# Performance work log

Measured on AMD Instinct MI355X. Metric: run time of the kernel, lower is better.

The kernel has to match this reference:

```python
import math
import jax, jax.numpy as jnp
import numpy as np

B_SZ, N_TOK, D_MODEL, EXPAND, D_STATE = 4, 1024, 192, 2, 16
D_INNER = EXPAND * D_MODEL  # 384


def setup_inputs() -> dict:
    key = jax.random.key(0)
    ks = jax.random.split(key, 6)
    dt_init = math.log(math.exp(0.1) - 1.0)
    x = jax.random.normal(ks[0], (B_SZ, N_TOK, D_INNER), dtype=jnp.float32)
    # dt projection weights: uniform(-1e-4, 1e-4), bias = softplus-inverse(0.1)
    W_dts = jax.random.uniform(ks[1], (D_INNER, D_INNER), minval=-1e-4, maxval=1e-4, dtype=jnp.float32)
    W_dtd = jax.random.uniform(ks[2], (D_INNER, D_INNER), minval=-1e-4, maxval=1e-4, dtype=jnp.float32)
    b_dts = jnp.full((D_INNER,), dt_init, dtype=jnp.float32)
    b_dtd = jnp.full((D_INNER,), dt_init, dtype=jnp.float32)
    # B/C projections (no bias)
    W_B = jax.random.normal(ks[3], (D_STATE, D_INNER), dtype=jnp.float32) * 0.05
    W_C = jax.random.normal(ks[4], (D_STATE, D_INNER), dtype=jnp.float32) * 0.05
    D_param = jnp.ones((D_INNER,), dtype=jnp.float32)
    A_log = jnp.broadcast_to(jnp.log(jnp.arange(1, D_STATE + 1, dtype=jnp.float32))[None, :], (D_INNER, D_STATE))
    diff_raw = jnp.zeros((1, D_INNER, 1, 1), dtype=jnp.float32)
    return {"x": x, "W_dts": W_dts, "b_dts": b_dts, "W_dtd": W_dtd, "b_dtd": b_dtd,
            "W_B": W_B, "W_C": W_C, "D_param": D_param, "A_log": A_log,
            "diff_raw": diff_raw, "K_steps": 3}


def _laplacian(h, H, W):
    # h: (B, N, D, S); 5-point stencil with replicate (edge) padding, per (D,S) channel
    Bv, N, D, S = h.shape
    g = h.reshape(Bv, H, W, D, S)
    g = jnp.pad(g, ((0, 0), (1, 1), (1, 1), (0, 0), (0, 0)), mode='edge')
    lap = (g[:, 2:, 1:-1] + g[:, :-2, 1:-1] + g[:, 1:-1, 2:] + g[:, 1:-1, :-2]
           - 4.0 * g[:, 1:-1, 1:-1])
    return lap.reshape(Bv, N, D, S)


def reference(x, W_dts, b_dts, W_dtd, b_dtd, W_B, W_C, D_param, A_log, diff_raw, K_steps):
    Bv, N, D = x.shape
    H = Wd = int(math.sqrt(N))
    A = -jax.nn.softplus(A_log)                                   # (D, S), negative decay
    delta_s = jnp.minimum(jax.nn.softplus(x @ W_dts.T + b_dts), 0.15)  # (B, N, D)
    delta_d = jnp.minimum(jax.nn.softplus(x @ W_dtd.T + b_dtd), 0.15)  # (B, N, D)
    B_mat = x @ W_B.T                                             # (B, N, S)
    C_mat = x @ W_C.T                                             # (B, N, S)
    h0 = jnp.einsum('bnd,bns->bnds', x, B_mat)                    # (B, N, D, S)
    D_coeff = (jax.nn.sigmoid(diff_raw) * 0.5).reshape(1, 1, D, 1)
    dt = 1.0 / K_steps
    A_exp = A[None, None]            # (1, 1, D, S)
    ds_e = delta_s[..., None]        # (B, N, D, 1)
    dd_e = delta_d[..., None]
    h = h0
    for _ in range(K_steps):
        lap = _laplacian(h, H, Wd)
        h = h + dt * (ds_e * (A_exp * h + h0) + dd_e * D_coeff * lap)
    y = jnp.einsum('bnds,bns->bnd', h, C_mat) + x * D_param
    return y
```

## Files before the change

### kernel.cpp

```cpp
#include <hip/hip_runtime.h>
#include <hip/hip_bf16.h>

#define BSZ   4
#define NTOK  1024
#define DIN   384
#define DST   16
#define MROWS (BSZ * NTOK)
#define KDIM  384
#define NM    (MROWS * DIN)

typedef __attribute__((ext_vector_type(8))) short bf16x8;
typedef __attribute__((ext_vector_type(4))) float f32x4;

__device__ __forceinline__ float softplus_f(float z) {
  return (z > 20.0f) ? z : log1pf(expf(z));
}

__device__ __forceinline__ unsigned short f32_to_bf16(float f) {
  unsigned int u = __float_as_uint(f);
  unsigned int rnd = 0x7fffu + ((u >> 16) & 1u);
  return (unsigned short)((u + rnd) >> 16);
}

__device__ __forceinline__ float bf16_lo(unsigned int w) { return __uint_as_float(w << 16); }
__device__ __forceinline__ float bf16_hi(unsigned int w) { return __uint_as_float(w & 0xffff0000u); }

__global__ __launch_bounds__(256) void wconv_kernel(
    const float* __restrict__ Wdts, const float* __restrict__ Wdtd,
    const float* __restrict__ WB,   const float* __restrict__ WC,
    unsigned short* __restrict__ Wb)
{
  const int idx8 = (blockIdx.x * 256 + threadIdx.x) * 8;
  const int row = idx8 / KDIM;
  const int k   = idx8 % KDIM;
  uint4 o = make_uint4(0u, 0u, 0u, 0u);
  if (row < 800) {
    const float* src;
    if (row < 384)      src = Wdts + (long)row * KDIM + k;
    else if (row < 768) src = Wdtd + (long)(row - 384) * KDIM + k;
    else if (row < 784) src = WB   + (long)(row - 768) * KDIM + k;
    else                src = WC   + (long)(row - 784) * KDIM + k;
    float4 v0 = *(const float4*)src;
    float4 v1 = *(const float4*)(src + 4);
    o.x = (unsigned int)f32_to_bf16(v0.x) | ((unsigned int)f32_to_bf16(v0.y) << 16);
    o.y = (unsigned int)f32_to_bf16(v0.z) | ((unsigned int)f32_to_bf16(v0.w) << 16);
    o.z = (unsigned int)f32_to_bf16(v1.x) | ((unsigned int)f32_to_bf16(v1.y) << 16);
    o.w = (unsigned int)f32_to_bf16(v1.z) | ((unsigned int)f32_to_bf16(v1.w) << 16);
  }
  *(uint4*)&Wb[idx8] = o;
}

__global__ __launch_bounds__(256) void xpose_kernel(
    const float* __restrict__ x, float* __restrict__ xT,
    unsigned short* __restrict__ xb)
{
  __shared__ float tile[32][33];
  const int n0 = blockIdx.x * 32;
  const int d0 = blockIdx.y * 32;
  const int b  = blockIdx.z;
  const int tx = threadIdx.x & 31, ty = threadIdx.x >> 5;
#pragma unroll
  for (int i = 0; i < 4; ++i) {
    int nn = n0 + ty + i * 8;
    float v = x[(long)(b * NTOK + nn) * DIN + d0 + tx];
    tile[ty + i * 8][tx] = v;
    xb[(long)(b * NTOK + nn) * DIN + d0 + tx] = f32_to_bf16(v);
  }
  __syncthreads();
#pragma unroll
  for (int i = 0; i < 4; ++i) {
    int dd = d0 + ty + i * 8;
    xT[(long)(b * DIN + dd) * NTOK + n0 + tx] = tile[tx][ty + i * 8];
  }
}

__global__ __launch_bounds__(256) void proj_mfma_kernel(
    const unsigned short* __restrict__ xb,
    const unsigned short* __restrict__ Wb,
    const float* __restrict__ bdts, const float* __restrict__ bdtd,
    unsigned short* __restrict__ dsT, unsigned short* __restrict__ ddT,
    float* __restrict__ BT, float* __restrict__ CT)
{
  __shared__ short smem_s[2][2][64 * 72];

  const int t    = threadIdx.x;
  const int bm   = blockIdx.x & 63;
  const int bn   = blockIdx.x >> 6;
  const int row0 = bm * 64;
  const int col0 = bn * 64;
  const int bat  = row0 >> 10;
  const int n0   = row0 & 1023;

  const int l  = t & 63;
  const int w  = t >> 6;
  const int wr = (w >> 1) * 32;
  const int wc = (w & 1) * 32;
  const int lr = l & 15;
  const int lk = (l >> 4) * 8;

  const int sr = t >> 2;
  const int sk = (t & 3) * 16;

  f32x4 acc[2][2];
  const f32x4 zero = {0.f, 0.f, 0.f, 0.f};
  acc[0][0] = zero; acc[0][1] = zero; acc[1][0] = zero; acc[1][1] = zero;

  uint4 la0, la1, lw0, lw1;
#define PLOAD(K0)                                                          \
  {                                                                        \
    const unsigned short* ap = &xb[(long)(row0 + sr) * KDIM + (K0) + sk];  \
    const unsigned short* wp = &Wb[(long)(col0 + sr) * KDIM + (K0) + sk];  \
    la0 = *(const uint4*)ap;  la1 = *(const uint4*)(ap + 8);               \
    lw0 = *(const uint4*)wp;  lw1 = *(const uint4*)(wp + 8);               \
  }
#define PSTORE(BUF)                                                        \
  {                                                                        \
    *(uint4*)&smem_s[BUF][0][sr * 72 + sk]     = la0;                      \
    *(uint4*)&smem_s[BUF][0][sr * 72 + sk + 8] = la1;                      \
    *(uint4*)&smem_s[BUF][1][sr * 72 + sk]     = lw0;                      \
    *(uint4*)&smem_s[BUF][1][sr * 72 + sk + 8] = lw1;                      \
  }

  PLOAD(0);
  PSTORE(0);

  for (int it = 0; it < 6; ++it) {
    const int cur = it & 1;
    __syncthreads();
    if (it + 1 < 6) PLOAD((it + 1) * 64);
    const short* Asm = smem_s[cur][0];
    const short* Wsm = smem_s[cur][1];
#pragma unroll
    for (int kh = 0; kh < 2; ++kh) {
      const int ko = kh * 32 + lk;
      bf16x8 a0 = *(const bf16x8*)&Asm[(wr + lr) * 72 + ko];
      bf16x8 a1 = *(const bf16x8*)&Asm[(wr + 16 + lr) * 72 + ko];
      bf16x8 b0 = *(const bf16x8*)&Wsm[(wc + lr) * 72 + ko];
      bf16x8 b1 = *(const bf16x8*)&Wsm[(wc + 16 + lr) * 72 + ko];
      acc[0][0] = __builtin_amdgcn_mfma_f32_16x16x32_bf16(a0, b0, acc[0][0], 0, 0, 0);
      acc[0][1] = __builtin_amdgcn_mfma_f32_16x16x32_bf16(a0, b1, acc[0][1], 0, 0, 0);
      acc[1][0] = __builtin_amdgcn_mfma_f32_16x16x32_bf16(a1, b0, acc[1][0], 0, 0, 0);
      acc[1][1] = __builtin_amdgcn_mfma_f32_16x16x32_bf16(a1, b1, acc[1][1], 0, 0, 0);
    }
    if (it + 1 < 6) PSTORE(cur ^ 1);
  }

  if (bn < 12) {
    const float* bias = (bn < 6) ? bdts : bdtd;
    unsigned short* plane = (bn < 6) ? dsT : ddT;
    const int dbase = (bn < 6) ? col0 : col0 - 384;
    const float bv0 = bias[dbase + wc + lr];
    const float bv1 = bias[dbase + wc + 16 + lr];
    __syncthreads();
    unsigned short* outl = (unsigned short*)smem_s;
#pragma unroll
    for (int i = 0; i < 2; ++i)
#pragma unroll
      for (int j = 0; j < 2; ++j) {
        const float bb = j ? bv1 : bv0;
        const int cl = wc + j * 16 + lr;
#pragma unroll
        for (int q = 0; q < 4; ++q) {
          const int nl = wr + i * 16 + (l >> 4) * 4 + q;
          float dl = fminf(softplus_f(acc[i][j][q] + bb), 0.15f);
          outl[cl * 72 + nl] = f32_to_bf16(dl);
        }
      }
    __syncthreads();
    const int dl = t >> 2;
    const int seg = t & 3;
    uint4 w0 = *(const uint4*)&outl[dl * 72 + seg * 16];
    uint4 w1 = *(const uint4*)&outl[dl * 72 + seg * 16 + 8];
    long addr = (long)(bat * DIN + dbase + dl) * NTOK + n0 + seg * 16;
    *(uint4*)&plane[addr]     = w0;
    *(uint4*)&plane[addr + 8] = w1;
  } else {
#pragma unroll
    for (int i = 0; i < 2; ++i)
#pragma unroll
      for (int j = 0; j < 2; ++j) {
        const int cl = wc + j * 16 + lr;
        const int rowbase = row0 + wr + i * 16 + (l >> 4) * 4;
        if (cl < 16)       *(f32x4*)&BT[(long)cl * MROWS + rowbase] = acc[i][j];
        else if (cl < 32)  *(f32x4*)&CT[(long)(cl - 16) * MROWS + rowbase] = acc[i][j];
      }
  }
#undef PLOAD
#undef PSTORE
}

__global__ __launch_bounds__(256) void ssm_kernel(
    const float* __restrict__ xT,
    const unsigned short* __restrict__ dsT,
    const unsigned short* __restrict__ ddT,
    const float* __restrict__ BT, const float* __restrict__ CT,
    const float* __restrict__ Alog,
    const float* __restrict__ diffraw, const int* __restrict__ Kp,
    unsigned short* __restrict__ yQ0, unsigned short* __restrict__ yQ1,
    unsigned short* __restrict__ yQ2, unsigned short* __restrict__ yQ3)
{
  __shared__ float P[4 * 1024];
  const int bid  = blockIdx.x;
  const int sq   = bid & 3;
  const int bd   = bid >> 2;
  const int d = bd % DIN;
  const int b = bd / DIN;
  const int t   = threadIdx.x;
  const int s   = sq * 4 + (t >> 6);
  const int l64 = t & 63;
  const int pr  = l64 >> 3, pc = l64 & 7;
  const int K = Kp[0];
  const float dt = 1.0f / (float)K;
  const float Dc = 0.5f / (1.0f + expf(-diffraw[d]));
  const float A  = -log1pf(expf(Alog[d * DST + s]));
  const float dtDc = dt * Dc;
  const long col = (long)(b * DIN + d) * NTOK;
  const long gr0 = (long)b * NTOK;
  const int  c0  = pc * 4;

  float h[16], cA[16], g0[16], a2v[16];
#pragma unroll
  for (int i = 0; i < 4; ++i) {
    const int n = (pr * 4 + i) * 32 + c0;
    float4 xv = *(const float4*)&xT[col + n];
    float4 bv = *(const float4*)&BT[(long)s * MROWS + gr0 + n];
    uint2 dsw = *(const uint2*)&dsT[col + n];
    uint2 ddw = *(const uint2*)&ddT[col + n];
    float dsf[4] = { bf16_lo(dsw.x), bf16_hi(dsw.x), bf16_lo(dsw.y), bf16_hi(dsw.y) };
    float ddf[4] = { bf16_lo(ddw.x), bf16_hi(ddw.x), bf16_lo(ddw.y), bf16_hi(ddw.y) };
    float xa[4] = { xv.x, xv.y, xv.z, xv.w };
    float ba[4] = { bv.x, bv.y, bv.z, bv.w };
#pragma unroll
    for (int j = 0; j < 4; ++j) {
      const int e = i * 4 + j;
      float a1 = dt * dsf[j];
      float a2 = dtDc * ddf[j];
      float h0 = xa[j] * ba[j];
      h[e]   = h0;
      g0[e]  = a1 * h0;
      a2v[e] = a2;
      cA[e]  = fmaf(a1, A, 1.0f) - 4.0f * a2;
    }
  }

  const int lu = (l64 - 8) & 63, ld = (l64 + 8) & 63;
  const int ll = (l64 - 1) & 63, lrr = (l64 + 1) & 63;

  for (int k = 0; k < K; ++k) {
    float up[4], dn[4], lf[4], rt[4];
#pragma unroll
    for (int j = 0; j < 4; ++j) {
      up[j] = __shfl(h[12 + j], lu);
      dn[j] = __shfl(h[j], ld);
      lf[j] = __shfl(h[4 * j + 3], ll);
      rt[j] = __shfl(h[4 * j], lrr);
    }
#pragma unroll
    for (int j = 0; j < 4; ++j) {
      up[j] = (pr == 0) ? h[j]          : up[j];
      dn[j] = (pr == 7) ? h[12 + j]     : dn[j];
      lf[j] = (pc == 0) ? h[4 * j]      : lf[j];
      rt[j] = (pc == 7) ? h[4 * j + 3]  : rt[j];
    }
    float hn[16];
#pragma unroll
    for (int i = 0; i < 4; ++i)
#pragma unroll
      for (int j = 0; j < 4; ++j) {
        const int e = i * 4 + j;
        float uv = (i == 0) ? up[j] : h[e - 4];
        float dv = (i == 3) ? dn[j] : h[e + 4];
        float lv = (j == 0) ? lf[i] : h[e - 1];
        float rv = (j == 3) ? rt[i] : h[e + 1];
        float S  = (uv + dv) + (lv + rv);
        hn[e] = fmaf(cA[e], h[e], fmaf(a2v[e], S, g0[e]));
      }
#pragma unroll
    for (int e = 0; e < 16; ++e) h[e] = hn[e];
  }

  const int sw = t >> 6;
#pragma unroll
  for (int i = 0; i < 4; ++i) {
    const int n = (pr * 4 + i) * 32 + c0;
    float4 cv = *(const float4*)&CT[(long)s * MROWS + gr0 + n];
    float4 pv;
    pv.x = h[i * 4 + 0] * cv.x;
    pv.y = h[i * 4 + 1] * cv.y;
    pv.z = h[i * 4 + 2] * cv.z;
    pv.w = h[i * 4 + 3] * cv.w;
    *(float4*)&P[sw * 1024 + n] = pv;
  }
  __syncthreads();

  unsigned short* yQ = (sq == 0) ? yQ0 : (sq == 1) ? yQ1 : (sq == 2) ? yQ2 : yQ3;
#pragma unroll
  for (int j = 0; j < 4; ++j) {
    const int n = t + j * 256;
    float sum = P[n] + P[1024 + n] + P[2048 + n] + P[3072 + n];
    yQ[col + n] = f32_to_bf16(sum);
  }
}

__global__ __launch_bounds__(256) void untranspose_kernel(
    const unsigned short* __restrict__ yQ0, const unsigned short* __restrict__ yQ1,
    const unsigned short* __restrict__ yQ2, const unsigned short* __restrict__ yQ3,
    const float* __restrict__ xT, const float* __restrict__ Dparam,
    float* __restrict__ out)
{
  __shared__ float tile[32][33];
  const int n0 = blockIdx.x * 32;
  const int d0 = blockIdx.y * 32;
  const int b  = blockIdx.z;
  const int tx = threadIdx.x & 31, ty = threadIdx.x >> 5;
#pragma unroll
  for (int i = 0; i < 4; ++i) {
    int dd = d0 + ty + i * 8;
    long idx = (long)(b * DIN + dd) * NTOK + n0 + tx;
    float v0 = __uint_as_float((unsigned int)yQ0[idx] << 16);
    float v1 = __uint_as_float((unsigned int)yQ1[idx] << 16);
    float v2 = __uint_as_float((unsigned int)yQ2[idx] << 16);
    float v3 = __uint_as_float((unsigned int)yQ3[idx] << 16);
    tile[ty + i * 8][tx] = ((v0 + v1) + (v2 + v3)) + xT[idx] * Dparam[dd];
  }
  __syncthreads();
#pragma unroll
  for (int i = 0; i < 4; ++i) {
    int nn = n0 + ty + i * 8;
    out[(long)(b * NTOK + nn) * DIN + d0 + tx] = tile[tx][ty + i * 8];
  }
}

extern "C" void kernel_launch(void* const* d_in, const int* in_sizes, int n_in,
                              void* d_out, int out_size, void* d_ws, size_t ws_size,
                              hipStream_t stream) {
  const float* x     = (const float*)d_in[0];
  const float* Wdts  = (const float*)d_in[1];
  const float* bdts  = (const float*)d_in[2];
  const float* Wdtd  = (const float*)d_in[3];
  const float* bdtd  = (const float*)d_in[4];
  const float* WB    = (const float*)d_in[5];
  const float* WC    = (const float*)d_in[6];
  const float* Dpar  = (const float*)d_in[7];
  const float* Alog  = (const float*)d_in[8];
  const float* diffr = (const float*)d_in[9];
  const int*   Kst   = (const int*)d_in[10];

  float* BT = (float*)d_ws;
  float* CT = BT + (long)DST * MROWS;
  float* xT = CT + (long)DST * MROWS;
  unsigned short* yQ0 = (unsigned short*)(xT + NM);
  unsigned short* yQ1 = yQ0 + NM;
  unsigned short* yQ2 = yQ1 + NM;
  unsigned short* yQ3 = yQ2 + NM;
  unsigned short* xb  = yQ0;
  unsigned short* Wb  = xb + NM;

  unsigned short* dsT = (unsigned short*)d_out;
  unsigned short* ddT = dsT + NM;

  wconv_kernel<<<dim3(156), dim3(256), 0, stream>>>(Wdts, Wdtd, WB, WC, Wb);

  xpose_kernel<<<dim3(NTOK / 32, DIN / 32, BSZ), dim3(256), 0, stream>>>(x, xT, xb);

  proj_mfma_kernel<<<dim3(64 * 13), dim3(256), 0, stream>>>(
      xb, Wb, bdts, bdtd, dsT, ddT, BT, CT);

  ssm_kernel<<<dim3(BSZ * DIN * 4), dim3(256), 0, stream>>>(
      xT, dsT, ddT, BT, CT, Alog, diffr, Kst, yQ0, yQ1, yQ2, yQ3);

  untranspose_kernel<<<dim3(NTOK / 32, DIN / 32, BSZ), dim3(256), 0, stream>>>(
      yQ0, yQ1, yQ2, yQ3, xT, Dpar, (float*)d_out);
}
```

Baseline: 66.84 us.

## Merge weight conversion into transpose kernel, reorder SSM blocks, prefetch C

Folds the weight bf16 conversion kernel into the x transpose kernel as an extra z-slice of blocks, removing one kernel launch and its serialization gap. The SSM kernel's block index mapping is changed so the state-quarter index is the slowest-varying dimension, which changes which blocks run concurrently and how their loads share the cache. The C-matrix loads are hoisted to the start of the SSM kernel so their latency overlaps the diffusion loop, at the cost of more live registers.

```diff
diff --git a/kernel.cpp b/kernel.cpp
--- a/kernel.cpp
+++ b/kernel.cpp
@@ -25,35 +25,36 @@
 __device__ __forceinline__ float bf16_lo(unsigned int w) { return __uint_as_float(w << 16); }
 __device__ __forceinline__ float bf16_hi(unsigned int w) { return __uint_as_float(w & 0xffff0000u); }
 
-__global__ __launch_bounds__(256) void wconv_kernel(
+__global__ __launch_bounds__(256) void prep_kernel(
+    const float* __restrict__ x, float* __restrict__ xT,
+    unsigned short* __restrict__ xb,
     const float* __restrict__ Wdts, const float* __restrict__ Wdtd,
     const float* __restrict__ WB,   const float* __restrict__ WC,
     unsigned short* __restrict__ Wb)
 {
-  const int idx8 = (blockIdx.x * 256 + threadIdx.x) * 8;
-  const int row = idx8 / KDIM;
-  const int k   = idx8 % KDIM;
-  uint4 o = make_uint4(0u, 0u, 0u, 0u);
-  if (row < 800) {
-    const float* src;
-    if (row < 384)      src = Wdts + (long)row * KDIM + k;
-    else if (row < 768) src = Wdtd + (long)(row - 384) * KDIM + k;
-    else if (row < 784) src = WB   + (long)(row - 768) * KDIM + k;
-    else                src = WC   + (long)(row - 784) * KDIM + k;
-    float4 v0 = *(const float4*)src;
-    float4 v1 = *(const float4*)(src + 4);
-    o.x = (unsigned int)f32_to_bf16(v0.x) | ((unsigned int)f32_to_bf16(v0.y) << 16);
-    o.y = (unsigned int)f32_to_bf16(v0.z) | ((unsigned int)f32_to_bf16(v0.w) << 16);
-    o.z = (unsigned int)f32_to_bf16(v1.x) | ((unsigned int)f32_to_bf16(v1.y) << 16);
-    o.w = (unsigned int)f32_to_bf16(v1.z) | ((unsigned int)f32_to_bf16(v1.w) << 16);
-  }
-  *(uint4*)&Wb[idx8] = o;
-}
-
-__global__ __launch_bounds__(256) void xpose_kernel(
-    const float* __restrict__ x, float* __restrict__ xT,
-    unsigned short* __restrict__ xb)
-{
+  if (blockIdx.z == 4) {
+    const int lin = blockIdx.y * 32 + blockIdx.x;
+    if (lin >= 156) return;
+    const int idx8 = (lin * 256 + threadIdx.x) * 8;
+    const int row = idx8 / KDIM;
+    const int k   = idx8 % KDIM;
+    uint4 o = make_uint4(0u, 0u, 0u, 0u);
+    if (row < 800) {
+      const float* src;
+      if (row < 384)      src = Wdts + (long)row * KDIM + k;
+      else if (row < 768) src = Wdtd + (long)(row - 384) * KDIM + k;
+      else if (row < 784) src = WB   + (long)(row - 768) * KDIM + k;
+      else                src = WC   + (long)(row - 784) * KDIM + k;
+      float4 v0 = *(const float4*)src;
+      float4 v1 = *(const float4*)(src + 4);
+      o.x = (unsigned int)f32_to_bf16(v0.x) | ((unsigned int)f32_to_bf16(v0.y) << 16);
+      o.y = (unsigned int)f32_to_bf16(v0.z) | ((unsigned int)f32_to_bf16(v0.w) << 16);
+      o.z = (unsigned int)f32_to_bf16(v1.x) | ((unsigned int)f32_to_bf16(v1.y) << 16);
+      o.w = (unsigned int)f32_to_bf16(v1.z) | ((unsigned int)f32_to_bf16(v1.w) << 16);
+    }
+    *(uint4*)&Wb[idx8] = o;
+    return;
+  }
   __shared__ float tile[32][33];
   const int n0 = blockIdx.x * 32;
   const int d0 = blockIdx.y * 32;
@@ -201,8 +202,8 @@
 {
   __shared__ float P[4 * 1024];
   const int bid  = blockIdx.x;
-  const int sq   = bid & 3;
-  const int bd   = bid >> 2;
+  const int sq   = bid / (BSZ * DIN);
+  const int bd   = bid % (BSZ * DIN);
   const int d = bd % DIN;
   const int b = bd / DIN;
   const int t   = threadIdx.x;
@@ -218,6 +219,11 @@
   const long gr0 = (long)b * NTOK;
   const int  c0  = pc * 4;
 
+  float4 cv[4];
+#pragma unroll
+  for (int i = 0; i < 4; ++i)
+    cv[i] = *(const float4*)&CT[(long)s * MROWS + gr0 + (pr * 4 + i) * 32 + c0];
+
   float h[16], cA[16], g0[16], a2v[16];
 #pragma unroll
   for (int i = 0; i < 4; ++i) {
@@ -283,12 +289,11 @@
 #pragma unroll
   for (int i = 0; i < 4; ++i) {
     const int n = (pr * 4 + i) * 32 + c0;
-    float4 cv = *(const float4*)&CT[(long)s * MROWS + gr0 + n];
     float4 pv;
-    pv.x = h[i * 4 + 0] * cv.x;
-    pv.y = h[i * 4 + 1] * cv.y;
-    pv.z = h[i * 4 + 2] * cv.z;
-    pv.w = h[i * 4 + 3] * cv.w;
+    pv.x = h[i * 4 + 0] * cv[i].x;
+    pv.y = h[i * 4 + 1] * cv[i].y;
+    pv.z = h[i * 4 + 2] * cv[i].z;
+    pv.w = h[i * 4 + 3] * cv[i].w;
     *(float4*)&P[sw * 1024 + n] = pv;
   }
   __syncthreads();
@@ -359,9 +364,8 @@
   unsigned short* dsT = (unsigned short*)d_out;
   unsigned short* ddT = dsT + NM;
 
-  wconv_kernel<<<dim3(156), dim3(256), 0, stream>>>(Wdts, Wdtd, WB, WC, Wb);
-
-  xpose_kernel<<<dim3(NTOK / 32, DIN / 32, BSZ), dim3(256), 0, stream>>>(x, xT, xb);
+  prep_kernel<<<dim3(NTOK / 32, DIN / 32, BSZ + 1), dim3(256), 0, stream>>>(
+      x, xT, xb, Wdts, Wdtd, WB, WC, Wb);
 
   proj_mfma_kernel<<<dim3(64 * 13), dim3(256), 0, stream>>>(
       xb, Wb, bdts, bdtd, dsT, ddT, BT, CT);
```

After: 63.72 us. 1.05x faster.
